# Kernel tuning notes

Measured on AMD Instinct MI355X. Metric: run time of the kernel, lower is better.

Reference implementation:

```python
import jax, jax.numpy as jnp
import numpy as np

HID = 1024
HEADS = 16
HEAD_DIM = HID // HEADS


def setup_inputs() -> dict:
    key = jax.random.key(0)
    ks = jax.random.split(key, 6)
    N, S = 4, 4096
    scale = 1.0 / np.sqrt(HID)
    return {
        "x": jax.random.normal(ks[0], (N, S, HID), dtype=jnp.float32),
        "Wq": jax.random.normal(ks[1], (HID, HID), dtype=jnp.float32) * scale,
        "Wk": jax.random.normal(ks[2], (HID, HID), dtype=jnp.float32) * scale,
        "Wv": jax.random.normal(ks[3], (HID, HID), dtype=jnp.float32) * scale,
        "Wo": jax.random.normal(ks[4], (HID, HID), dtype=jnp.float32) * scale,
        "bo": jnp.zeros((HID,), dtype=jnp.float32),
    }


def reference(x, Wq, Wk, Wv, Wo, bo):
    N, S, _ = x.shape
    # Linear projections (torch Linear: y = x @ W^T; here W stored as [in, out])
    q = (x @ Wq).reshape(N, S, HEADS, HEAD_DIM)
    k = (x @ Wk).reshape(N, S, HEADS, HEAD_DIM)
    v = (x @ Wv).reshape(N, S, HEADS, HEAD_DIM)
    # transpose(1,2): [N, H, S, D]
    q = jnp.swapaxes(q, 1, 2)
    k = jnp.swapaxes(k, 1, 2)
    v = jnp.swapaxes(v, 1, 2)
    # Faithful to source: einsum labels 'nqhd,nkhd->nqk' applied to [N,H,S,D]
    # tensors => contracts over (seq, head_dim); energy is [N, H, H].
    energy = jnp.einsum('nahd,nbhd->nab', q, k)  # a,b index heads; h indexes seq
    attention = jax.nn.softmax(energy / np.sqrt(HEAD_DIM), axis=2)  # [N, H, H]
    # 'nqk,nkhd->nqhd' on [N,H,H] x [N,H,S,D] -> [N,H,S,D]
    out = jnp.einsum('nab,nbsd->nasd', attention, v)
    # Faithful reshape (mixes head/seq axes exactly as torch .reshape does)
    out = out.reshape(N, S, HID)
    return out @ Wo + bo
```

## Files before the change

### kernel.cpp

```cpp
#include <hip/hip_runtime.h>
#include <hip/hip_bf16.h>

#define HID 1024
#define SEQ 4096
#define NBATCH 4

typedef __attribute__((ext_vector_type(8))) short bf16x8;
typedef __attribute__((ext_vector_type(4))) float f32x4;

__device__ __forceinline__ unsigned short f2bf(float f) {
  union { float f; unsigned u; } v; v.f = f;
  unsigned r = v.u + 0x7fffu + ((v.u >> 16) & 1u);
  return (unsigned short)(r >> 16);
}
__device__ __forceinline__ float bf2f(unsigned short h) {
  union { unsigned u; float f; } v; v.u = ((unsigned)h) << 16; return v.f;
}
__device__ __forceinline__ void gload16(const void* g, void* l) {
  __builtin_amdgcn_global_load_lds(
      (const __attribute__((address_space(1))) unsigned*)g,
      (__attribute__((address_space(3))) unsigned*)l, 16, 0, 0);
}

__global__ __launch_bounds__(256) void split_x_kernel(
    const float* __restrict__ x, unsigned short* __restrict__ xhi,
    unsigned short* __restrict__ xlo) {
  const int i = blockIdx.x * 256 + threadIdx.x;
  const float4 v = ((const float4*)x)[i];
  const float f[4] = {v.x, v.y, v.z, v.w};
  unsigned short hh[4], ll[4];
#pragma unroll
  for (int j = 0; j < 4; ++j) {
    const unsigned short hb = f2bf(f[j]);
    hh[j] = hb;
    ll[j] = f2bf(f[j] - bf2f(hb));
  }
  ushort4 h, l;
  h.x = hh[0]; h.y = hh[1]; h.z = hh[2]; h.w = hh[3];
  l.x = ll[0]; l.y = ll[1]; l.z = ll[2]; l.w = ll[3];
  ((ushort4*)xhi)[i] = h;
  ((ushort4*)xlo)[i] = l;
}

__global__ __launch_bounds__(256) void split_w_kernel(
    const float* __restrict__ Wq, const float* __restrict__ Wk,
    const float* __restrict__ Wv, const float* __restrict__ Wo,
    unsigned short* qh, unsigned short* ql, unsigned short* kh,
    unsigned short* kl, unsigned short* vh, unsigned short* oh) {
  const float* W; unsigned short* dh; unsigned short* dl;
  if (blockIdx.z == 0)      { W = Wq; dh = qh; dl = ql; }
  else if (blockIdx.z == 1) { W = Wk; dh = kh; dl = kl; }
  else if (blockIdx.z == 2) { W = Wv; dh = vh; dl = nullptr; }
  else                      { W = Wo; dh = oh; dl = nullptr; }
  __shared__ float t[32][33];
  const int tx = threadIdx.x & 31, ty = threadIdx.x >> 5;
  const int c0 = blockIdx.x * 32, r0 = blockIdx.y * 32;
#pragma unroll
  for (int i = 0; i < 32; i += 8)
    t[ty + i][tx] = W[(size_t)(r0 + ty + i) * HID + c0 + tx];
  __syncthreads();
#pragma unroll
  for (int i = 0; i < 32; i += 8) {
    const float f = t[tx][ty + i];
    const size_t di = (size_t)(c0 + ty + i) * HID + (r0 + tx);
    const unsigned short hb = f2bf(f);
    dh[di] = hb;
    if (dl) dl[di] = f2bf(f - bf2f(hb));
  }
}

template <bool SPLIT3, bool OUT_BF16, bool BIAS>
__global__ __launch_bounds__(256, 2) void gemm_kernel(
    const unsigned short* __restrict__ A1, const unsigned short* __restrict__ A2,
    const unsigned short* __restrict__ B1, const unsigned short* __restrict__ B2,
    float* __restrict__ Cf, unsigned short* __restrict__ Cb,
    const float* __restrict__ bias, int M, int N, int Kd) {
  constexpr int TILE = 128 * 32;
  constexpr int NT = SPLIT3 ? 4 : 2;
  __shared__ unsigned short lds[NT * TILE];
  unsigned short* As1 = lds;
  unsigned short* Bs1 = lds + TILE;
  unsigned short* As2 = SPLIT3 ? lds + 2 * TILE : nullptr;
  unsigned short* Bs2 = SPLIT3 ? lds + 3 * TILE : nullptr;

  const int tid = threadIdx.x;
  const int lane = tid & 63;
  const int w = tid >> 6;
  const int wr = w >> 1, wc = w & 1;
  const int m0 = blockIdx.x * 128, n0 = blockIdx.y * 128;
  const int z = blockIdx.z;

  const unsigned short* pA1 = A1 + (size_t)z * M * Kd;
  const unsigned short* pA2 = SPLIT3 ? A2 + (size_t)z * M * Kd : nullptr;

  f32x4 acc[4][4] = {};

  const int fr = lane & 15;
  const int k8 = (lane >> 4) * 8;

  for (int kt = 0; kt < Kd; kt += 32) {
#pragma unroll
    for (int i = 0; i < 2; ++i) {
      const int ob = i * 4096 + tid * 16;
      const int r = ob >> 6;
      const int ce = (ob & 63) >> 1;
      gload16(pA1 + (size_t)(m0 + r) * Kd + kt + ce, (char*)As1 + ob);
      gload16(B1 + (size_t)(n0 + r) * Kd + kt + ce, (char*)Bs1 + ob);
      if (SPLIT3) {
        gload16(pA2 + (size_t)(m0 + r) * Kd + kt + ce, (char*)As2 + ob);
        gload16(B2 + (size_t)(n0 + r) * Kd + kt + ce, (char*)Bs2 + ob);
      }
    }
    __syncthreads();
    bf16x8 a1[4], b1[4], a2[4], b2[4];
#pragma unroll
    for (int m = 0; m < 4; ++m) {
      const int row = wr * 64 + m * 16 + fr;
      a1[m] = *(const bf16x8*)&As1[row * 32 + k8];
      if (SPLIT3) a2[m] = *(const bf16x8*)&As2[row * 32 + k8];
    }
#pragma unroll
    for (int n = 0; n < 4; ++n) {
      const int row = wc * 64 + n * 16 + fr;
      b1[n] = *(const bf16x8*)&Bs1[row * 32 + k8];
      if (SPLIT3) b2[n] = *(const bf16x8*)&Bs2[row * 32 + k8];
    }
#pragma unroll
    for (int m = 0; m < 4; ++m)
#pragma unroll
      for (int n = 0; n < 4; ++n) {
        acc[m][n] = __builtin_amdgcn_mfma_f32_16x16x32_bf16(a1[m], b1[n], acc[m][n], 0, 0, 0);
        if (SPLIT3) {
          acc[m][n] = __builtin_amdgcn_mfma_f32_16x16x32_bf16(a1[m], b2[n], acc[m][n], 0, 0, 0);
          acc[m][n] = __builtin_amdgcn_mfma_f32_16x16x32_bf16(a2[m], b1[n], acc[m][n], 0, 0, 0);
        }
      }
    __syncthreads();
  }

  const int r4 = (lane >> 4) * 4;
#pragma unroll
  for (int m = 0; m < 4; ++m) {
    const int row0 = m0 + wr * 64 + m * 16 + r4;
#pragma unroll
    for (int n = 0; n < 4; ++n) {
      const int col = n0 + wc * 64 + n * 16 + fr;
      const float bv = BIAS ? bias[col] : 0.0f;
#pragma unroll
      for (int r2 = 0; r2 < 4; ++r2) {
        const size_t idx = (size_t)z * M * N + (size_t)(row0 + r2) * N + col;
        const float vv = acc[m][n][r2] + bv;
        if (OUT_BF16) Cb[idx] = f2bf(vv);
        else Cf[idx] = vv;
      }
    }
  }
}

__global__ __launch_bounds__(256) void energy_kernel(
    const float* __restrict__ Q, const float* __restrict__ Kq,
    float* __restrict__ energy) {
  const int n = blockIdx.y;
  const int s0 = blockIdx.x * 32;
  __shared__ float qs[16 * 68];
  __shared__ float ks[16 * 68];
  const int tid = threadIdx.x;
  const int a = tid >> 4, b = tid & 15;
  const int hb = (tid * 4) >> 6, d0 = (tid * 4) & 63;
  const float* Qn = Q + (size_t)n * SEQ * HID;
  const float* Kn = Kq + (size_t)n * SEQ * HID;
  float acc = 0.0f;
  for (int s = s0; s < s0 + 32; ++s) {
    __syncthreads();
    const float4 q4 = ((const float4*)(Qn + (size_t)s * HID))[tid];
    const float4 k4 = ((const float4*)(Kn + (size_t)s * HID))[tid];
    float* qp = qs + hb * 68 + d0;
    qp[0] = q4.x; qp[1] = q4.y; qp[2] = q4.z; qp[3] = q4.w;
    float* kp = ks + hb * 68 + d0;
    kp[0] = k4.x; kp[1] = k4.y; kp[2] = k4.z; kp[3] = k4.w;
    __syncthreads();
    float dot = 0.0f;
#pragma unroll
    for (int d = 0; d < 64; ++d) dot += qs[a * 68 + d] * ks[b * 68 + d];
    acc += dot;
  }
  atomicAdd(&energy[n * 256 + a * 16 + b], acc);
}

__global__ void softmax_kernel(const float* __restrict__ energy,
                               float* __restrict__ att) {
  const int t = threadIdx.x;
  const float* e = energy + t * 16;
  float m = -3.0e38f;
#pragma unroll
  for (int b = 0; b < 16; ++b) m = fmaxf(m, e[b]);
  float p[16];
  float ssum = 0.0f;
#pragma unroll
  for (int b = 0; b < 16; ++b) { p[b] = expf((e[b] - m) * 0.125f); ssum += p[b]; }
  const float inv = 1.0f / ssum;
#pragma unroll
  for (int b = 0; b < 16; ++b) att[t * 16 + b] = p[b] * inv;
}

__global__ __launch_bounds__(256) void out2_kernel(
    const unsigned short* __restrict__ V, const float* __restrict__ att,
    unsigned short* __restrict__ out2) {
  const int n = blockIdx.y, sg = blockIdx.x;
  __shared__ unsigned short vl[16 * 1032];
  __shared__ float al[256];
  const int tid = threadIdx.x;
  al[tid] = att[n * 256 + tid];
  const unsigned short* Vbp = V + ((size_t)n * SEQ + (size_t)sg * 16) * HID;
#pragma unroll
  for (int j = 0; j < 16; ++j) {
    const ushort4 u = *(const ushort4*)(Vbp + (size_t)j * HID + tid * 4);
    *(ushort4*)&vl[j * 1032 + tid * 4] = u;
  }
  __syncthreads();
  const int c0 = tid * 4;
  const int rr = c0 >> 6, d = c0 & 63;
  float vb[16][4];
#pragma unroll
  for (int b = 0; b < 16; ++b)
#pragma unroll
    for (int j = 0; j < 4; ++j)
      vb[b][j] = bf2f(vl[rr * 1032 + b * 64 + d + j]);
#pragma unroll
  for (int h = 0; h < 16; ++h) {
    float o0 = 0, o1 = 0, o2 = 0, o3 = 0;
#pragma unroll
    for (int b = 0; b < 16; ++b) {
      const float wgt = al[h * 16 + b];
      o0 += wgt * vb[b][0]; o1 += wgt * vb[b][1];
      o2 += wgt * vb[b][2]; o3 += wgt * vb[b][3];
    }
    ushort4 u;
    u.x = f2bf(o0); u.y = f2bf(o1); u.z = f2bf(o2); u.w = f2bf(o3);
    *(ushort4*)(out2 + ((size_t)n * SEQ + (size_t)(h * 256 + sg)) * HID + c0) = u;
  }
}

extern "C" void kernel_launch(void* const* d_in, const int* in_sizes, int n_in,
                              void* d_out, int out_size, void* d_ws, size_t ws_size,
                              hipStream_t stream) {
  (void)in_sizes; (void)n_in; (void)out_size; (void)ws_size;
  const float* x  = (const float*)d_in[0];
  const float* Wq = (const float*)d_in[1];
  const float* Wk = (const float*)d_in[2];
  const float* Wv = (const float*)d_in[3];
  const float* Wo = (const float*)d_in[4];
  const float* bo = (const float*)d_in[5];
  float* out = (float*)d_out;

  char* ws = (char*)d_ws;
  size_t off = 0;
  auto alloc = [&](size_t bytes) {
    char* p = ws + off;
    off += (bytes + 255) & ~(size_t)255;
    return p;
  };
  const size_t XE = (size_t)NBATCH * SEQ * HID;
  unsigned short* Xhi = (unsigned short*)alloc(XE * 2);
  unsigned short* Xlo = (unsigned short*)alloc(XE * 2);
  unsigned short* WqhT = (unsigned short*)alloc((size_t)HID * HID * 2);
  unsigned short* WqlT = (unsigned short*)alloc((size_t)HID * HID * 2);
  unsigned short* WkhT = (unsigned short*)alloc((size_t)HID * HID * 2);
  unsigned short* WklT = (unsigned short*)alloc((size_t)HID * HID * 2);
  unsigned short* WvhT = (unsigned short*)alloc((size_t)HID * HID * 2);
  unsigned short* WohT = (unsigned short*)alloc((size_t)HID * HID * 2);
  float* Q  = (float*)alloc(XE * 4);
  float* Kf = (float*)alloc(XE * 4);
  float* energy = (float*)alloc((size_t)NBATCH * 256 * 4);
  float* att    = (float*)alloc((size_t)NBATCH * 256 * 4);
  unsigned short* Vb = (unsigned short*)Xlo;
  unsigned short* O2 = (unsigned short*)Q;

  split_x_kernel<<<(unsigned)(XE / 4 / 256), 256, 0, stream>>>(x, Xhi, Xlo);
  split_w_kernel<<<dim3(HID / 32, HID / 32, 4), 256, 0, stream>>>(
      Wq, Wk, Wv, Wo, WqhT, WqlT, WkhT, WklT, WvhT, WohT);

  dim3 gg(SEQ / 128, HID / 128, NBATCH);
  gemm_kernel<true, false, false><<<gg, 256, 0, stream>>>(
      Xhi, Xlo, WqhT, WqlT, Q, nullptr, nullptr, SEQ, HID, HID);
  gemm_kernel<true, false, false><<<gg, 256, 0, stream>>>(
      Xhi, Xlo, WkhT, WklT, Kf, nullptr, nullptr, SEQ, HID, HID);
  gemm_kernel<false, true, false><<<gg, 256, 0, stream>>>(
      Xhi, nullptr, WvhT, nullptr, nullptr, Vb, nullptr, SEQ, HID, HID);

  hipMemsetAsync(energy, 0, (size_t)NBATCH * 256 * 4, stream);
  energy_kernel<<<dim3(SEQ / 32, NBATCH), 256, 0, stream>>>(Q, Kf, energy);
  softmax_kernel<<<1, 64, 0, stream>>>(energy, att);
  out2_kernel<<<dim3(256, NBATCH), 256, 0, stream>>>(Vb, att, O2);

  gemm_kernel<false, false, true><<<gg, 256, 0, stream>>>(
      O2, nullptr, WohT, nullptr, out, nullptr, bo, SEQ, HID, HID);
}
```

Baseline: 468.2 us.

## Compute energy via per-batch Gram matrix instead of full Q and K projections

Reassociates the energy contraction so it uses G = X^T X per batch (1024x1024). M1 = G·Wq is then contracted against Wk, which replaces the two large SEQxHID Q and K projection GEMMs with a split-K Gram GEMM, a reduction, and a small HIDxHID GEMM. The x split kernel now also writes a transposed hi/lo copy for the Gram computation, and the K weight split is dropped. This removes the fp32 Q/K intermediates and a large share of the GEMM FLOPs. In exchange it adds a transpose pass and changes the rounding path through the Gram matrix.

```diff
diff --git a/kernel.cpp b/kernel.cpp
--- a/kernel.cpp
+++ b/kernel.cpp
@@ -24,33 +24,37 @@
 
 __global__ __launch_bounds__(256) void split_x_kernel(
     const float* __restrict__ x, unsigned short* __restrict__ xhi,
-    unsigned short* __restrict__ xlo) {
-  const int i = blockIdx.x * 256 + threadIdx.x;
-  const float4 v = ((const float4*)x)[i];
-  const float f[4] = {v.x, v.y, v.z, v.w};
-  unsigned short hh[4], ll[4];
-#pragma unroll
-  for (int j = 0; j < 4; ++j) {
-    const unsigned short hb = f2bf(f[j]);
-    hh[j] = hb;
-    ll[j] = f2bf(f[j] - bf2f(hb));
-  }
-  ushort4 h, l;
-  h.x = hh[0]; h.y = hh[1]; h.z = hh[2]; h.w = hh[3];
-  l.x = ll[0]; l.y = ll[1]; l.z = ll[2]; l.w = ll[3];
-  ((ushort4*)xhi)[i] = h;
-  ((ushort4*)xlo)[i] = l;
+    unsigned short* __restrict__ xthi, unsigned short* __restrict__ xtlo) {
+  const int n = blockIdx.z;
+  const int c0 = blockIdx.x * 32;
+  const int s0 = blockIdx.y * 32;
+  __shared__ float t[32][33];
+  const int tx = threadIdx.x & 31, ty = threadIdx.x >> 5;
+  const float* xp = x + (size_t)n * SEQ * HID;
+#pragma unroll
+  for (int i = 0; i < 32; i += 8) {
+    const float f = xp[(size_t)(s0 + ty + i) * HID + c0 + tx];
+    t[ty + i][tx] = f;
+    xhi[(size_t)n * SEQ * HID + (size_t)(s0 + ty + i) * HID + c0 + tx] = f2bf(f);
+  }
+  __syncthreads();
+#pragma unroll
+  for (int i = 0; i < 32; i += 8) {
+    const float f = t[tx][ty + i];
+    const size_t di = (size_t)n * HID * SEQ + (size_t)(c0 + ty + i) * SEQ + s0 + tx;
+    const unsigned short hb = f2bf(f);
+    xthi[di] = hb;
+    xtlo[di] = f2bf(f - bf2f(hb));
+  }
 }
 
 __global__ __launch_bounds__(256) void split_w_kernel(
-    const float* __restrict__ Wq, const float* __restrict__ Wk,
-    const float* __restrict__ Wv, const float* __restrict__ Wo,
-    unsigned short* qh, unsigned short* ql, unsigned short* kh,
-    unsigned short* kl, unsigned short* vh, unsigned short* oh) {
+    const float* __restrict__ Wq, const float* __restrict__ Wv,
+    const float* __restrict__ Wo, unsigned short* qh, unsigned short* ql,
+    unsigned short* vh, unsigned short* oh) {
   const float* W; unsigned short* dh; unsigned short* dl;
   if (blockIdx.z == 0)      { W = Wq; dh = qh; dl = ql; }
-  else if (blockIdx.z == 1) { W = Wk; dh = kh; dl = kl; }
-  else if (blockIdx.z == 2) { W = Wv; dh = vh; dl = nullptr; }
+  else if (blockIdx.z == 1) { W = Wv; dh = vh; dl = nullptr; }
   else                      { W = Wo; dh = oh; dl = nullptr; }
   __shared__ float t[32][33];
   const int tx = threadIdx.x & 31, ty = threadIdx.x >> 5;
@@ -157,9 +161,105 @@
   }
 }
 
+__global__ __launch_bounds__(256, 2) void gram_kernel(
+    const unsigned short* __restrict__ Xthi, const unsigned short* __restrict__ Xtlo,
+    float* __restrict__ Gpart) {
+  constexpr int TILE = 128 * 32;
+  __shared__ unsigned short lds[4 * TILE];
+  unsigned short* As1 = lds;
+  unsigned short* Bs1 = lds + TILE;
+  unsigned short* As2 = lds + 2 * TILE;
+  unsigned short* Bs2 = lds + 3 * TILE;
+
+  const int tid = threadIdx.x;
+  const int lane = tid & 63;
+  const int w = tid >> 6;
+  const int wr = w >> 1, wc = w & 1;
+  const int m0 = blockIdx.x * 128, n0 = blockIdx.y * 128;
+  const int nb = blockIdx.z >> 1, chunk = blockIdx.z & 1;
+
+  const size_t abase = (size_t)nb * HID * SEQ + (size_t)chunk * 2048;
+  const unsigned short* pH = Xthi + abase;
+  const unsigned short* pL = Xtlo + abase;
+
+  f32x4 acc[4][4] = {};
+  const int fr = lane & 15;
+  const int k8 = (lane >> 4) * 8;
+
+  for (int kt = 0; kt < 2048; kt += 32) {
+#pragma unroll
+    for (int i = 0; i < 2; ++i) {
+      const int ob = i * 4096 + tid * 16;
+      const int r = ob >> 6;
+      const int ce = (ob & 63) >> 1;
+      gload16(pH + (size_t)(m0 + r) * SEQ + kt + ce, (char*)As1 + ob);
+      gload16(pH + (size_t)(n0 + r) * SEQ + kt + ce, (char*)Bs1 + ob);
+      gload16(pL + (size_t)(m0 + r) * SEQ + kt + ce, (char*)As2 + ob);
+      gload16(pL + (size_t)(n0 + r) * SEQ + kt + ce, (char*)Bs2 + ob);
+    }
+    __syncthreads();
+    bf16x8 a1[4], b1[4], a2[4], b2[4];
+#pragma unroll
+    for (int m = 0; m < 4; ++m) {
+      const int row = wr * 64 + m * 16 + fr;
+      a1[m] = *(const bf16x8*)&As1[row * 32 + k8];
+      a2[m] = *(const bf16x8*)&As2[row * 32 + k8];
+    }
+#pragma unroll
+    for (int n = 0; n < 4; ++n) {
+      const int row = wc * 64 + n * 16 + fr;
+      b1[n] = *(const bf16x8*)&Bs1[row * 32 + k8];
+      b2[n] = *(const bf16x8*)&Bs2[row * 32 + k8];
+    }
+#pragma unroll
+    for (int m = 0; m < 4; ++m)
+#pragma unroll
+      for (int n = 0; n < 4; ++n) {
+        acc[m][n] = __builtin_amdgcn_mfma_f32_16x16x32_bf16(a1[m], b1[n], acc[m][n], 0, 0, 0);
+        acc[m][n] = __builtin_amdgcn_mfma_f32_16x16x32_bf16(a1[m], b2[n], acc[m][n], 0, 0, 0);
+        acc[m][n] = __builtin_amdgcn_mfma_f32_16x16x32_bf16(a2[m], b1[n], acc[m][n], 0, 0, 0);
+      }
+    __syncthreads();
+  }
+
+  float* Cf = Gpart + ((size_t)chunk * NBATCH + nb) * HID * HID;
+  const int r4 = (lane >> 4) * 4;
+#pragma unroll
+  for (int m = 0; m < 4; ++m) {
+    const int row0 = m0 + wr * 64 + m * 16 + r4;
+#pragma unroll
+    for (int n = 0; n < 4; ++n) {
+      const int col = n0 + wc * 64 + n * 16 + fr;
+#pragma unroll
+      for (int r2 = 0; r2 < 4; ++r2)
+        Cf[(size_t)(row0 + r2) * HID + col] = acc[m][n][r2];
+    }
+  }
+}
+
+__global__ __launch_bounds__(256) void reduce_split_kernel(
+    const float* __restrict__ Gp, unsigned short* __restrict__ ghi,
+    unsigned short* __restrict__ glo) {
+  const size_t i = ((size_t)blockIdx.x * 256 + threadIdx.x) * 4;
+  const float4 a = *(const float4*)(Gp + i);
+  const float4 b = *(const float4*)(Gp + i + (size_t)NBATCH * HID * HID);
+  const float f[4] = {a.x + b.x, a.y + b.y, a.z + b.z, a.w + b.w};
+  ushort4 h, l;
+  unsigned short hh[4], ll[4];
+#pragma unroll
+  for (int j = 0; j < 4; ++j) {
+    hh[j] = f2bf(f[j]);
+    ll[j] = f2bf(f[j] - bf2f(hh[j]));
+  }
+  h.x = hh[0]; h.y = hh[1]; h.z = hh[2]; h.w = hh[3];
+  l.x = ll[0]; l.y = ll[1]; l.z = ll[2]; l.w = ll[3];
+  *(ushort4*)(ghi + i) = h;
+  *(ushort4*)(glo + i) = l;
+}
+
 __global__ __launch_bounds__(256) void energy_kernel(
     const float* __restrict__ Q, const float* __restrict__ Kq,
-    float* __restrict__ energy) {
+    float* __restrict__ energy, size_t qstride, size_t kstride) {
   const int n = blockIdx.y;
   const int s0 = blockIdx.x * 32;
   __shared__ float qs[16 * 68];
@@ -167,8 +267,8 @@
   const int tid = threadIdx.x;
   const int a = tid >> 4, b = tid & 15;
   const int hb = (tid * 4) >> 6, d0 = (tid * 4) & 63;
-  const float* Qn = Q + (size_t)n * SEQ * HID;
-  const float* Kn = Kq + (size_t)n * SEQ * HID;
+  const float* Qn = Q + (size_t)n * qstride;
+  const float* Kn = Kq + (size_t)n * kstride;
   float acc = 0.0f;
   for (int s = s0; s < s0 + 32; ++s) {
     __syncthreads();
@@ -261,38 +361,45 @@
     return p;
   };
   const size_t XE = (size_t)NBATCH * SEQ * HID;
-  unsigned short* Xhi = (unsigned short*)alloc(XE * 2);
-  unsigned short* Xlo = (unsigned short*)alloc(XE * 2);
+  const size_t GE = (size_t)NBATCH * HID * HID;
+  unsigned short* Xhi  = (unsigned short*)alloc(XE * 2);
+  unsigned short* Xthi = (unsigned short*)alloc(XE * 2);
+  unsigned short* Xtlo = (unsigned short*)alloc(XE * 2);
   unsigned short* WqhT = (unsigned short*)alloc((size_t)HID * HID * 2);
   unsigned short* WqlT = (unsigned short*)alloc((size_t)HID * HID * 2);
-  unsigned short* WkhT = (unsigned short*)alloc((size_t)HID * HID * 2);
-  unsigned short* WklT = (unsigned short*)alloc((size_t)HID * HID * 2);
   unsigned short* WvhT = (unsigned short*)alloc((size_t)HID * HID * 2);
   unsigned short* WohT = (unsigned short*)alloc((size_t)HID * HID * 2);
-  float* Q  = (float*)alloc(XE * 4);
-  float* Kf = (float*)alloc(XE * 4);
+  float* Gpart = (float*)alloc(2 * GE * 4);
+  unsigned short* Ghi = (unsigned short*)alloc(GE * 2);
+  unsigned short* Glo = (unsigned short*)alloc(GE * 2);
   float* energy = (float*)alloc((size_t)NBATCH * 256 * 4);
   float* att    = (float*)alloc((size_t)NBATCH * 256 * 4);
-  unsigned short* Vb = (unsigned short*)Xlo;
-  unsigned short* O2 = (unsigned short*)Q;
-
-  split_x_kernel<<<(unsigned)(XE / 4 / 256), 256, 0, stream>>>(x, Xhi, Xlo);
-  split_w_kernel<<<dim3(HID / 32, HID / 32, 4), 256, 0, stream>>>(
-      Wq, Wk, Wv, Wo, WqhT, WqlT, WkhT, WklT, WvhT, WohT);
-
-  dim3 gg(SEQ / 128, HID / 128, NBATCH);
-  gemm_kernel<true, false, false><<<gg, 256, 0, stream>>>(
-      Xhi, Xlo, WqhT, WqlT, Q, nullptr, nullptr, SEQ, HID, HID);
-  gemm_kernel<true, false, false><<<gg, 256, 0, stream>>>(
-      Xhi, Xlo, WkhT, WklT, Kf, nullptr, nullptr, SEQ, HID, HID);
-  gemm_kernel<false, true, false><<<gg, 256, 0, stream>>>(
+  unsigned short* Vb = Xthi;
+  float* M1 = Gpart;
+  unsigned short* O2 = Xtlo;
+
+  split_x_kernel<<<dim3(HID / 32, SEQ / 32, NBATCH), 256, 0, stream>>>(
+      x, Xhi, Xthi, Xtlo);
+  split_w_kernel<<<dim3(HID / 32, HID / 32, 3), 256, 0, stream>>>(
+      Wq, Wv, Wo, WqhT, WqlT, WvhT, WohT);
+
+  gram_kernel<<<dim3(HID / 128, HID / 128, NBATCH * 2), 256, 0, stream>>>(
+      Xthi, Xtlo, Gpart);
+  reduce_split_kernel<<<(unsigned)(GE / 4 / 256), 256, 0, stream>>>(
+      Gpart, Ghi, Glo);
+
+  gemm_kernel<false, true, false><<<dim3(SEQ / 128, HID / 128, NBATCH), 256, 0, stream>>>(
       Xhi, nullptr, WvhT, nullptr, nullptr, Vb, nullptr, SEQ, HID, HID);
 
+  gemm_kernel<true, false, false><<<dim3(HID / 128, HID / 128, NBATCH), 256, 0, stream>>>(
+      Ghi, Glo, WqhT, WqlT, M1, nullptr, nullptr, HID, HID, HID);
+
   hipMemsetAsync(energy, 0, (size_t)NBATCH * 256 * 4, stream);
-  energy_kernel<<<dim3(SEQ / 32, NBATCH), 256, 0, stream>>>(Q, Kf, energy);
+  energy_kernel<<<dim3(HID / 32, NBATCH), 256, 0, stream>>>(
+      M1, Wk, energy, (size_t)HID * HID, 0);
   softmax_kernel<<<1, 64, 0, stream>>>(energy, att);
   out2_kernel<<<dim3(256, NBATCH), 256, 0, stream>>>(Vb, att, O2);
 
-  gemm_kernel<false, false, true><<<gg, 256, 0, stream>>>(
+  gemm_kernel<false, false, true><<<dim3(SEQ / 128, HID / 128, NBATCH), 256, 0, stream>>>(
       O2, nullptr, WohT, nullptr, out, nullptr, bo, SEQ, HID, HID);
 }
```

Result: faster. 439.9 us (-6.0%).
